# Performance work log

Measured on AMD Instinct MI355X. Metric: run time of the kernel, lower is better.

## Reference

```python
import jax, jax.numpy as jnp
import numpy as np

DIM = 512
N_HEADS = 8
HEAD_DIM = DIM // N_HEADS


def rope_pos(T, head_dim, dtype=jnp.float32):
    inv_freq = 1.0 / (10000.0 ** (jnp.arange(0, head_dim, 2, dtype=jnp.float32) / head_dim))
    t = jnp.arange(T, dtype=jnp.float32)
    freqs = jnp.einsum('i,j->ij', t, inv_freq)            # [T, head_dim/2]
    return jnp.concatenate([freqs, freqs], axis=-1).astype(dtype)  # [T, head_dim]


def rotate_half(x):
    x1, x2 = jnp.split(x, 2, axis=-1)
    return jnp.concatenate([-x2, x1], axis=-1)


def apply_rope(pos, t):
    # pos: [T, hd] -> broadcast to [1,1,T,hd]; t: [B,H,T,hd]
    pos = pos[None, None, :, :]
    return t * jnp.cos(pos) + rotate_half(t) * jnp.sin(pos)


def setup_inputs() -> dict:
    key = jax.random.key(0)
    ks = jax.random.split(key, 6)
    B, T = 4, 2048
    x = jax.random.normal(ks[0], (B, T, DIM), dtype=jnp.float32)
    mask = jnp.zeros((B, T), dtype=jnp.float32)  # additive mask
    s = 1.0 / np.sqrt(DIM)
    qkv_w = jax.random.normal(ks[1], (3 * DIM, DIM), dtype=jnp.float32) * s
    qkv_b = jnp.zeros((3 * DIM,), dtype=jnp.float32)
    proj_w = jax.random.normal(ks[2], (DIM, DIM), dtype=jnp.float32) * s
    proj_b = jnp.zeros((DIM,), dtype=jnp.float32)
    return {"x": x, "mask": mask, "qkv_w": qkv_w, "qkv_b": qkv_b,
            "proj_w": proj_w, "proj_b": proj_b}


def reference(x, mask, qkv_w, qkv_b, proj_w, proj_b):
    B, T, C = x.shape
    qkv = x @ qkv_w.T + qkv_b                       # [B,T,3C]
    qkv = qkv.reshape(B, T, 3, N_HEADS, HEAD_DIM)
    q, k, v = qkv[:, :, 0], qkv[:, :, 1], qkv[:, :, 2]  # [B,T,H,hd]
    q = q.transpose(0, 2, 1, 3)                     # [B,H,T,hd]
    k = k.transpose(0, 2, 1, 3)
    v = v.transpose(0, 2, 1, 3)
    pos = rope_pos(T, HEAD_DIM, x.dtype)
    q = apply_rope(pos, q)
    k = apply_rope(pos, k)
    scores = jnp.einsum('bhqd,bhkd->bhqk', q, k) * (1.0 / np.sqrt(HEAD_DIM))
    scores = scores + mask[:, None, None, :]        # 2D mask -> [B,1,1,T]
    probs = jax.nn.softmax(scores.astype(jnp.float32), axis=-1).astype(x.dtype)
    # dropout is identity in eval mode
    out = jnp.einsum('bhqk,bhkd->bhqd', probs, v)   # [B,H,T,hd]
    out = out.transpose(0, 2, 1, 3).reshape(B, T, C)
    return out @ proj_w.T + proj_b
```

## Files before the change

### kernel.cpp

```cpp
#include <hip/hip_runtime.h>
#include <math.h>


typedef __attribute__((ext_vector_type(8))) short bf16x8;
typedef __attribute__((ext_vector_type(4))) float floatx4;

#define LOG2E 1.44269504088896f
#define MAX3(a, b, c) fmaxf(fmaxf((a), (b)), (c))

__device__ __forceinline__ unsigned short f2bf(float f) {
  unsigned int u = __float_as_uint(f);
  u += 0x7fffu + ((u >> 16) & 1u);
  return (unsigned short)(u >> 16);
}

__device__ __forceinline__ unsigned int cvtpk_bf16(float a, float b) {
  unsigned int r;
  asm("v_cvt_pk_bf16_f32 %0, %1, %2" : "=v"(r) : "v"(a), "v"(b));
  return r;
}

__device__ __forceinline__ void gld_lds16(unsigned short* lds, const unsigned short* g) {
  __builtin_amdgcn_global_load_lds(
      (const __attribute__((address_space(1))) unsigned int*)g,
      (__attribute__((address_space(3))) unsigned int*)lds, 16, 0, 0);
}

__global__ __launch_bounds__(256) void prep_kernel(
    const float* __restrict__ x, const float* __restrict__ wq, const float* __restrict__ wp,
    const float* __restrict__ mask,
    unsigned short* __restrict__ xb, unsigned short* __restrict__ wqb,
    unsigned short* __restrict__ wpb, float* __restrict__ cosT, float* __restrict__ sinT,
    float* __restrict__ maskE) {
  int i = blockIdx.x * 256 + threadIdx.x;
  if (i < 655360) {
    int base = i * 8;
    const float* src;
    unsigned short* dst;
    int j;
    if (base < 4194304)      { src = x;  dst = xb;  j = base; }
    else if (base < 4980736) { src = wq; dst = wqb; j = base - 4194304; }
    else                     { src = wp; dst = wpb; j = base - 4980736; }
    float4 a = *(const float4*)(src + j);
    float4 b = *(const float4*)(src + j + 4);
    uint4 r;
    r.x = cvtpk_bf16(a.x, a.y);
    r.y = cvtpk_bf16(a.z, a.w);
    r.z = cvtpk_bf16(b.x, b.y);
    r.w = cvtpk_bf16(b.z, b.w);
    *(uint4*)(dst + j) = r;
  } else if (i < 720896) {
    int j = i - 655360;
    int t = j >> 5, f = j & 31;
    double fr = (double)t * pow(10000.0, -(double)f / 32.0);
    cosT[j] = (float)cos(fr);
    sinT[j] = (float)sin(fr);
  } else if (i < 721920) {
    int j = (i - 720896) * 8;
    float4 a = *(const float4*)(mask + j);
    float4 b = *(const float4*)(mask + j + 4);
    a.x *= LOG2E; a.y *= LOG2E; a.z *= LOG2E; a.w *= LOG2E;
    b.x *= LOG2E; b.y *= LOG2E; b.z *= LOG2E; b.w *= LOG2E;
    *(float4*)(maskE + j) = a;
    *(float4*)(maskE + j + 4) = b;
  }
}

__global__ __launch_bounds__(256) void qkv_kernel(
    const unsigned short* __restrict__ xb, const unsigned short* __restrict__ wqb,
    const float* __restrict__ qkv_b, const float* __restrict__ cosT,
    const float* __restrict__ sinT, unsigned short* __restrict__ Qb,
    unsigned short* __restrict__ Kb, unsigned short* __restrict__ Vtb) {
  __shared__ __align__(16) unsigned short SM[2][2][128 * 32];
  const int tid = threadIdx.x;
  const int wave = tid >> 6, lane = tid & 63, ln = lane & 15, quad = lane >> 4;
  const int m0 = blockIdx.x * 128, n0 = blockIdx.y * 128;
  const int wr = (wave >> 1) * 64, wc = (wave & 1) * 64;

  floatx4 acc[4][4];
#pragma unroll
  for (int i = 0; i < 4; ++i)
#pragma unroll
    for (int j = 0; j < 4; ++j) acc[i][j] = (floatx4){0.f, 0.f, 0.f, 0.f};

  const int c0 = tid, c1 = tid + 256;
  const int ar0 = c0 >> 2, ak0 = (c0 & 3) * 8;
  const int ar1 = c1 >> 2, ak1 = (c1 & 3) * 8;

  gld_lds16(SM[0][0] + c0 * 8, xb + (size_t)(m0 + ar0) * 512 + ak0);
  gld_lds16(SM[0][0] + c1 * 8, xb + (size_t)(m0 + ar1) * 512 + ak1);
  gld_lds16(SM[0][1] + c0 * 8, wqb + (size_t)(n0 + ar0) * 512 + ak0);
  gld_lds16(SM[0][1] + c1 * 8, wqb + (size_t)(n0 + ar1) * 512 + ak1);
  __syncthreads();

  for (int kt = 0; kt < 16; ++kt) {
    const int cur = kt & 1;
    if (kt < 15) {
      const int kn = (kt + 1) * 32;
      gld_lds16(SM[cur ^ 1][0] + c0 * 8, xb + (size_t)(m0 + ar0) * 512 + kn + ak0);
      gld_lds16(SM[cur ^ 1][0] + c1 * 8, xb + (size_t)(m0 + ar1) * 512 + kn + ak1);
      gld_lds16(SM[cur ^ 1][1] + c0 * 8, wqb + (size_t)(n0 + ar0) * 512 + kn + ak0);
      gld_lds16(SM[cur ^ 1][1] + c1 * 8, wqb + (size_t)(n0 + ar1) * 512 + kn + ak1);
    }
    bf16x8 af[4], bfb[4];
#pragma unroll
    for (int mi = 0; mi < 4; ++mi)
      af[mi] = *(const bf16x8*)(SM[cur][0] + (wr + mi * 16 + ln) * 32 + quad * 8);
#pragma unroll
    for (int ni = 0; ni < 4; ++ni)
      bfb[ni] = *(const bf16x8*)(SM[cur][1] + (wc + ni * 16 + ln) * 32 + quad * 8);
#pragma unroll
    for (int mi = 0; mi < 4; ++mi)
#pragma unroll
      for (int ni = 0; ni < 4; ++ni)
        acc[mi][ni] = __builtin_amdgcn_mfma_f32_16x16x32_bf16(af[mi], bfb[ni], acc[mi][ni], 0, 0, 0);
    __syncthreads();
  }

  const int colbase = n0 + wc;
  const int mat = colbase >> 9;
  float bias[4];
#pragma unroll
  for (int ni = 0; ni < 4; ++ni) bias[ni] = qkv_b[colbase + ni * 16 + ln];

  unsigned short* Ls = &SM[0][0][0];
  const int bidx = m0 >> 11, tl0 = m0 & 2047;
  const int h0 = (n0 & 511) >> 6;

  if (mat == 2) {
#pragma unroll
    for (int mi = 0; mi < 4; ++mi) {
      int r0 = wr + mi * 16 + quad * 4;
#pragma unroll
      for (int ni = 0; ni < 4; ++ni) {
        int c = wc + ni * 16 + ln;
        ushort4 pk;
        pk.x = f2bf(acc[mi][ni][0] + bias[ni]);
        pk.y = f2bf(acc[mi][ni][1] + bias[ni]);
        pk.z = f2bf(acc[mi][ni][2] + bias[ni]);
        pk.w = f2bf(acc[mi][ni][3] + bias[ni]);
        *(ushort4*)(Ls + c * 128 + (r0 ^ ((c & 7) << 3))) = pk;
      }
    }
    __syncthreads();
    const int j2 = tid & 15, rid = tid >> 4;
#pragma unroll
    for (int it = 0; it < 8; ++it) {
      int c = it * 16 + rid;
      int hh = c >> 6, dd = c & 63;
      uint4 v = *(const uint4*)(Ls + c * 128 + ((j2 * 8) ^ ((c & 7) << 3)));
      *(uint4*)(Vtb + ((size_t)(bidx * 8 + h0 + hh) * 64 + dd) * 2048 + tl0 + j2 * 8) = v;
    }
  } else {
    unsigned short* dst = (mat == 0) ? Qb : Kb;
    const float sc = (mat == 0) ? 0.125f * LOG2E : 1.0f;
#pragma unroll
    for (int mi = 0; mi < 4; ++mi) {
#pragma unroll
      for (int r = 0; r < 4; ++r) {
        int lr = wr + mi * 16 + quad * 4 + r;
        int t = tl0 + lr;
        const float* cr = cosT + t * 32;
        const float* sr = sinT + t * 32;
        int xr = (lr & 7) << 3;
#pragma unroll
        for (int ni = 0; ni < 2; ++ni) {
          int dlo = ni * 16 + ln;
          float cv = cr[dlo], sv = sr[dlo];
          float xlo = acc[mi][ni][r] + bias[ni];
          float xhi = acc[mi][ni + 2][r] + bias[ni + 2];
          Ls[lr * 128 + ((wc + dlo) ^ xr)]      = f2bf((xlo * cv - xhi * sv) * sc);
          Ls[lr * 128 + ((wc + dlo + 32) ^ xr)] = f2bf((xhi * cv + xlo * sv) * sc);
        }
      }
    }
    __syncthreads();
    const int jj = tid & 7, rowid = tid >> 3;
#pragma unroll
    for (int it = 0; it < 8; ++it) {
      int hr = it * 32 + rowid;
      int rr = hr & 127, hh = hr >> 7;
      int c = hh * 64 + jj * 8;
      uint4 v = *(const uint4*)(Ls + rr * 128 + (c ^ ((rr & 7) << 3)));
      *(uint4*)(dst + ((size_t)(bidx * 8 + h0 + hh) * 2048 + tl0 + rr) * 64 + jj * 8) = v;
    }
  }
}

__global__ __launch_bounds__(512) void attn_kernel(
    const unsigned short* __restrict__ Qb, const unsigned short* __restrict__ Kb,
    const unsigned short* __restrict__ Vtb, const float* __restrict__ maskE,
    unsigned short* __restrict__ attnb) {
  __shared__ __align__(16) unsigned short Ks[2][64 * 64];
  __shared__ __align__(16) unsigned short Vs[2][64 * 64];
  __shared__ __align__(16) unsigned short Ps[128 * 64];

  const int tid = threadIdx.x;
  const int wave = tid >> 6, lane = tid & 63, ln = lane & 15, quad = lane >> 4;
  const int swz = (ln & 7) << 3;
  const int bh = blockIdx.y;
  const int b = bh >> 3, h = bh & 7;
  const int q0 = blockIdx.x * 128;
  const int wq = wave * 16;

  const unsigned short* Qhead = Qb + (size_t)bh * 2048 * 64;
  const unsigned short* Khead = Kb + (size_t)bh * 2048 * 64;
  const unsigned short* Vhead = Vtb + (size_t)bh * 64 * 2048;

  bf16x8 qf[2];
#pragma unroll
  for (int ks = 0; ks < 2; ++ks)
    qf[ks] = *(const bf16x8*)(Qhead + (size_t)(q0 + wq + ln) * 64 + ks * 32 + quad * 8);

  floatx4 o[4];
#pragma unroll
  for (int mi2 = 0; mi2 < 4; ++mi2) o[mi2] = (floatx4){0.f, 0.f, 0.f, 0.f};
  float mrun = -INFINITY;
  float lrun = 0.f;

  const int srow = tid >> 3;
  const int gcol = (((tid & 7) ^ (srow & 7)) << 3);
  const unsigned short* ksrc = Khead + (size_t)srow * 64 + gcol;
  const unsigned short* vsrc = Vhead + (size_t)srow * 2048 + gcol;
  unsigned short* kdst0 = Ks[0] + tid * 8;
  unsigned short* vdst0 = Vs[0] + tid * 8;
  unsigned short* kdst1 = Ks[1] + tid * 8;
  unsigned short* vdst1 = Vs[1] + tid * 8;

  gld_lds16(kdst0, ksrc);
  gld_lds16(vdst0, vsrc);
  __syncthreads();

  for (int kt = 0; kt < 32; ++kt) {
    const int cur = kt & 1;
    const int k0 = kt * 64;
    if (kt < 31) {
      gld_lds16(cur ? kdst0 : kdst1, ksrc + (size_t)(k0 + 64) * 64);
      gld_lds16(cur ? vdst0 : vdst1, vsrc + k0 + 64);
    }

    floatx4 sm[4];
    __builtin_amdgcn_s_setprio(1);
#pragma unroll
    for (int mi = 0; mi < 4; ++mi) {
      bf16x8 kf0 = *(const bf16x8*)(Ks[cur] + (mi * 16 + ln) * 64 + ((quad * 8) ^ swz));
      bf16x8 kf1 = *(const bf16x8*)(Ks[cur] + (mi * 16 + ln) * 64 + ((32 + quad * 8) ^ swz));
      floatx4 a = (floatx4){0.f, 0.f, 0.f, 0.f};
      a = __builtin_amdgcn_mfma_f32_16x16x32_bf16(kf0, qf[0], a, 0, 0, 0);
      a = __builtin_amdgcn_mfma_f32_16x16x32_bf16(kf1, qf[1], a, 0, 0, 0);
      sm[mi] = a;
    }
    __builtin_amdgcn_s_setprio(0);
#pragma unroll
    for (int mi = 0; mi < 4; ++mi) {
      float4 mv = *(const float4*)(maskE + b * 2048 + k0 + mi * 16 + quad * 4);
      sm[mi][0] += mv.x; sm[mi][1] += mv.y;
      sm[mi][2] += mv.z; sm[mi][3] += mv.w;
    }
    float t0 = MAX3(sm[0][0], sm[0][1], sm[0][2]);
    float t1 = MAX3(sm[0][3], sm[1][0], sm[1][1]);
    float t2 = MAX3(sm[1][2], sm[1][3], sm[2][0]);
    float t3 = MAX3(sm[2][1], sm[2][2], sm[2][3]);
    float t4 = MAX3(sm[3][0], sm[3][1], sm[3][2]);
    float vmax = fmaxf(MAX3(t0, t1, t2), MAX3(t3, t4, sm[3][3]));
    vmax = fmaxf(vmax, __shfl_xor(vmax, 16));
    vmax = fmaxf(vmax, __shfl_xor(vmax, 32));
    if (__any(vmax > mrun)) {
      float nm = fmaxf(mrun, vmax);
      float alpha = exp2f(mrun - nm);
      mrun = nm;
      lrun *= alpha;
#pragma unroll
      for (int mi2 = 0; mi2 < 4; ++mi2) {
        o[mi2][0] *= alpha; o[mi2][1] *= alpha;
        o[mi2][2] *= alpha; o[mi2][3] *= alpha;
      }
    }
    float ps[4];
#pragma unroll
    for (int mi = 0; mi < 4; ++mi) {
      float p0 = exp2f(sm[mi][0] - mrun);
      float p1 = exp2f(sm[mi][1] - mrun);
      float p2 = exp2f(sm[mi][2] - mrun);
      float p3 = exp2f(sm[mi][3] - mrun);
      sm[mi][0] = p0; sm[mi][1] = p1; sm[mi][2] = p2; sm[mi][3] = p3;
      ps[mi] = (p0 + p1) + (p2 + p3);
    }
    float psum = (ps[0] + ps[1]) + (ps[2] + ps[3]);
    psum += __shfl_xor(psum, 16);
    psum += __shfl_xor(psum, 32);
    lrun += psum;

#pragma unroll
    for (int mi = 0; mi < 4; ++mi) {
      uint2 pk;
      pk.x = cvtpk_bf16(sm[mi][0], sm[mi][1]);
      pk.y = cvtpk_bf16(sm[mi][2], sm[mi][3]);
      *(uint2*)(Ps + (wq + ln) * 64 + ((mi * 16 + quad * 4) ^ swz)) = pk;
    }
    __builtin_amdgcn_s_setprio(1);
#pragma unroll
    for (int ks = 0; ks < 2; ++ks) {
      bf16x8 pb = *(const bf16x8*)(Ps + (wq + ln) * 64 + ((ks * 32 + quad * 8) ^ swz));
#pragma unroll
      for (int mi2 = 0; mi2 < 4; ++mi2) {
        bf16x8 vf = *(const bf16x8*)(Vs[cur] + (mi2 * 16 + ln) * 64 + ((ks * 32 + quad * 8) ^ swz));
        o[mi2] = __builtin_amdgcn_mfma_f32_16x16x32_bf16(vf, pb, o[mi2], 0, 0, 0);
      }
    }
    __builtin_amdgcn_s_setprio(0);

    __syncthreads();
  }

  {
    float inv = 1.f / lrun;
    int t = q0 + wq + ln;
    size_t base = ((size_t)b * 2048 + t) * 512 + h * 64;
#pragma unroll
    for (int mi2 = 0; mi2 < 4; ++mi2) {
      uint2 pk;
      pk.x = cvtpk_bf16(o[mi2][0] * inv, o[mi2][1] * inv);
      pk.y = cvtpk_bf16(o[mi2][2] * inv, o[mi2][3] * inv);
      *(uint2*)(attnb + base + mi2 * 16 + quad * 4) = pk;
    }
  }
}

__global__ __launch_bounds__(512) void proj_kernel(
    const unsigned short* __restrict__ ab, const unsigned short* __restrict__ wpb,
    const float* __restrict__ proj_b, float* __restrict__ out) {
  __shared__ __align__(16) unsigned short As[2][128 * 32];
  __shared__ __align__(16) unsigned short Bs[2][128 * 32];
  const int tid = threadIdx.x;
  const int wave = tid >> 6, lane = tid & 63, ln = lane & 15, quad = lane >> 4;
  const int m0 = blockIdx.x * 128, n0 = blockIdx.y * 128;
  const int wr = (wave >> 1) * 32, wc = (wave & 1) * 64;

  floatx4 acc[2][4];
#pragma unroll
  for (int i = 0; i < 2; ++i)
#pragma unroll
    for (int j = 0; j < 4; ++j) acc[i][j] = (floatx4){0.f, 0.f, 0.f, 0.f};

  const int ar = tid >> 2, ak = (tid & 3) * 8;

  gld_lds16(As[0] + tid * 8, ab + (size_t)(m0 + ar) * 512 + ak);
  gld_lds16(Bs[0] + tid * 8, wpb + (size_t)(n0 + ar) * 512 + ak);
  __syncthreads();

  for (int kt = 0; kt < 16; ++kt) {
    const int cur = kt & 1;
    if (kt < 15) {
      const int kn = (kt + 1) * 32;
      gld_lds16(As[cur ^ 1] + tid * 8, ab + (size_t)(m0 + ar) * 512 + kn + ak);
      gld_lds16(Bs[cur ^ 1] + tid * 8, wpb + (size_t)(n0 + ar) * 512 + kn + ak);
    }
    bf16x8 af[2], bfb[4];
#pragma unroll
    for (int mi = 0; mi < 2; ++mi)
      af[mi] = *(const bf16x8*)(As[cur] + (wr + mi * 16 + ln) * 32 + quad * 8);
#pragma unroll
    for (int ni = 0; ni < 4; ++ni)
      bfb[ni] = *(const bf16x8*)(Bs[cur] + (wc + ni * 16 + ln) * 32 + quad * 8);
#pragma unroll
    for (int mi = 0; mi < 2; ++mi)
#pragma unroll
      for (int ni = 0; ni < 4; ++ni)
        acc[mi][ni] = __builtin_amdgcn_mfma_f32_16x16x32_bf16(af[mi], bfb[ni], acc[mi][ni], 0, 0, 0);
    __syncthreads();
  }

#pragma unroll
  for (int mi = 0; mi < 2; ++mi)
#pragma unroll
    for (int ni = 0; ni < 4; ++ni) {
      int col = n0 + wc + ni * 16 + ln;
      float pb = proj_b[col];
#pragma unroll
      for (int r = 0; r < 4; ++r) {
        int row = m0 + wr + mi * 16 + quad * 4 + r;
        out[(size_t)row * 512 + col] = acc[mi][ni][r] + pb;
      }
    }
}

extern "C" void kernel_launch(void* const* d_in, const int* in_sizes, int n_in,
                              void* d_out, int out_size, void* d_ws, size_t ws_size,
                              hipStream_t stream) {
  const float* x      = (const float*)d_in[0];
  const float* mask   = (const float*)d_in[1];
  const float* qkv_w  = (const float*)d_in[2];
  const float* qkv_b  = (const float*)d_in[3];
  const float* proj_w = (const float*)d_in[4];
  const float* proj_b = (const float*)d_in[5];
  float* out = (float*)d_out;

  char* ws = (char*)d_ws;
  unsigned short* xb   = (unsigned short*)(ws);
  unsigned short* wqb  = (unsigned short*)(ws + 8388608);
  unsigned short* wpb  = (unsigned short*)(ws + 9961472);
  float* cosT          = (float*)(ws + 10485760);
  float* sinT          = (float*)(ws + 10747904);
  unsigned short* Qb   = (unsigned short*)(ws + 11010048);
  unsigned short* Kb   = (unsigned short*)(ws + 19398656);
  unsigned short* Vtb  = (unsigned short*)(ws + 27787264);
  unsigned short* attnb= (unsigned short*)(ws + 36175872);
  float* maskE         = (float*)(ws + 44564480);

  prep_kernel<<<2820, 256, 0, stream>>>(x, qkv_w, proj_w, mask, xb, wqb, wpb, cosT, sinT, maskE);
  dim3 g1(64, 12);
  qkv_kernel<<<g1, 256, 0, stream>>>(xb, wqb, qkv_b, cosT, sinT, Qb, Kb, Vtb);
  dim3 g2(16, 32);
  attn_kernel<<<g2, 512, 0, stream>>>(Qb, Kb, Vtb, maskE, attnb);
  dim3 g3(64, 4);
  proj_kernel<<<g3, 512, 0, stream>>>(attnb, wpb, proj_b, out);
}
```

Measured before the change: 187.1 us.

## Give each attention wave 32 query rows and register-staged K/V prefetch

```diff
diff --git a/kernel.cpp b/kernel.cpp
--- a/kernel.cpp
+++ b/kernel.cpp
@@ -187,7 +187,7 @@
   }
 }
 
-__global__ __launch_bounds__(512) void attn_kernel(
+__global__ __launch_bounds__(256) void attn_kernel(
     const unsigned short* __restrict__ Qb, const unsigned short* __restrict__ Kb,
     const unsigned short* __restrict__ Vtb, const float* __restrict__ maskE,
     unsigned short* __restrict__ attnb) {
@@ -201,127 +201,166 @@
   const int bh = blockIdx.y;
   const int b = bh >> 3, h = bh & 7;
   const int q0 = blockIdx.x * 128;
-  const int wq = wave * 16;
+  const int wq = wave * 32;
 
   const unsigned short* Qhead = Qb + (size_t)bh * 2048 * 64;
   const unsigned short* Khead = Kb + (size_t)bh * 2048 * 64;
   const unsigned short* Vhead = Vtb + (size_t)bh * 64 * 2048;
 
-  bf16x8 qf[2];
-#pragma unroll
-  for (int ks = 0; ks < 2; ++ks)
-    qf[ks] = *(const bf16x8*)(Qhead + (size_t)(q0 + wq + ln) * 64 + ks * 32 + quad * 8);
-
-  floatx4 o[4];
-#pragma unroll
-  for (int mi2 = 0; mi2 < 4; ++mi2) o[mi2] = (floatx4){0.f, 0.f, 0.f, 0.f};
-  float mrun = -INFINITY;
-  float lrun = 0.f;
+  bf16x8 qf[2][2];
+#pragma unroll
+  for (int ni2 = 0; ni2 < 2; ++ni2)
+#pragma unroll
+    for (int ks = 0; ks < 2; ++ks)
+      qf[ni2][ks] = *(const bf16x8*)(Qhead + (size_t)(q0 + wq + ni2 * 16 + ln) * 64 + ks * 32 + quad * 8);
+
+  floatx4 o[4][2];
+#pragma unroll
+  for (int mi2 = 0; mi2 < 4; ++mi2)
+#pragma unroll
+    for (int ni2 = 0; ni2 < 2; ++ni2) o[mi2][ni2] = (floatx4){0.f, 0.f, 0.f, 0.f};
+  float mrun[2] = {-INFINITY, -INFINITY};
+  float lrun[2] = {0.f, 0.f};
 
   const int srow = tid >> 3;
-  const int gcol = (((tid & 7) ^ (srow & 7)) << 3);
-  const unsigned short* ksrc = Khead + (size_t)srow * 64 + gcol;
-  const unsigned short* vsrc = Vhead + (size_t)srow * 2048 + gcol;
-  unsigned short* kdst0 = Ks[0] + tid * 8;
-  unsigned short* vdst0 = Vs[0] + tid * 8;
-  unsigned short* kdst1 = Ks[1] + tid * 8;
-  unsigned short* vdst1 = Vs[1] + tid * 8;
-
-  gld_lds16(kdst0, ksrc);
-  gld_lds16(vdst0, vsrc);
+  const int scol = (tid & 7) * 8;
+  const int sx = scol ^ ((srow & 7) << 3);
+  const int sd0 = srow * 64 + sx, sd1 = (srow + 32) * 64 + sx;
+
+  {
+    uint4 k0a = *(const uint4*)(Khead + (size_t)srow * 64 + scol);
+    uint4 k0b = *(const uint4*)(Khead + (size_t)(srow + 32) * 64 + scol);
+    uint4 v0a = *(const uint4*)(Vhead + (size_t)srow * 2048 + scol);
+    uint4 v0b = *(const uint4*)(Vhead + (size_t)(srow + 32) * 2048 + scol);
+    *(uint4*)(Ks[0] + sd0) = k0a;
+    *(uint4*)(Ks[0] + sd1) = k0b;
+    *(uint4*)(Vs[0] + sd0) = v0a;
+    *(uint4*)(Vs[0] + sd1) = v0b;
+  }
   __syncthreads();
 
   for (int kt = 0; kt < 32; ++kt) {
     const int cur = kt & 1;
     const int k0 = kt * 64;
+    uint4 kpa, kpb, vpa, vpb;
     if (kt < 31) {
-      gld_lds16(cur ? kdst0 : kdst1, ksrc + (size_t)(k0 + 64) * 64);
-      gld_lds16(cur ? vdst0 : vdst1, vsrc + k0 + 64);
-    }
-
-    floatx4 sm[4];
-    __builtin_amdgcn_s_setprio(1);
+      kpa = *(const uint4*)(Khead + (size_t)(k0 + 64 + srow) * 64 + scol);
+      kpb = *(const uint4*)(Khead + (size_t)(k0 + 64 + srow + 32) * 64 + scol);
+      vpa = *(const uint4*)(Vhead + (size_t)srow * 2048 + k0 + 64 + scol);
+      vpb = *(const uint4*)(Vhead + (size_t)(srow + 32) * 2048 + k0 + 64 + scol);
+    }
+
+    floatx4 sm[4][2];
 #pragma unroll
     for (int mi = 0; mi < 4; ++mi) {
       bf16x8 kf0 = *(const bf16x8*)(Ks[cur] + (mi * 16 + ln) * 64 + ((quad * 8) ^ swz));
       bf16x8 kf1 = *(const bf16x8*)(Ks[cur] + (mi * 16 + ln) * 64 + ((32 + quad * 8) ^ swz));
-      floatx4 a = (floatx4){0.f, 0.f, 0.f, 0.f};
-      a = __builtin_amdgcn_mfma_f32_16x16x32_bf16(kf0, qf[0], a, 0, 0, 0);
-      a = __builtin_amdgcn_mfma_f32_16x16x32_bf16(kf1, qf[1], a, 0, 0, 0);
-      sm[mi] = a;
-    }
-    __builtin_amdgcn_s_setprio(0);
+#pragma unroll
+      for (int ni2 = 0; ni2 < 2; ++ni2) {
+        floatx4 a = (floatx4){0.f, 0.f, 0.f, 0.f};
+        a = __builtin_amdgcn_mfma_f32_16x16x32_bf16(kf0, qf[ni2][0], a, 0, 0, 0);
+        a = __builtin_amdgcn_mfma_f32_16x16x32_bf16(kf1, qf[ni2][1], a, 0, 0, 0);
+        sm[mi][ni2] = a;
+      }
+    }
 #pragma unroll
     for (int mi = 0; mi < 4; ++mi) {
       float4 mv = *(const float4*)(maskE + b * 2048 + k0 + mi * 16 + quad * 4);
-      sm[mi][0] += mv.x; sm[mi][1] += mv.y;
-      sm[mi][2] += mv.z; sm[mi][3] += mv.w;
-    }
-    float t0 = MAX3(sm[0][0], sm[0][1], sm[0][2]);
-    float t1 = MAX3(sm[0][3], sm[1][0], sm[1][1]);
-    float t2 = MAX3(sm[1][2], sm[1][3], sm[2][0]);
-    float t3 = MAX3(sm[2][1], sm[2][2], sm[2][3]);
-    float t4 = MAX3(sm[3][0], sm[3][1], sm[3][2]);
-    float vmax = fmaxf(MAX3(t0, t1, t2), MAX3(t3, t4, sm[3][3]));
-    vmax = fmaxf(vmax, __shfl_xor(vmax, 16));
-    vmax = fmaxf(vmax, __shfl_xor(vmax, 32));
-    if (__any(vmax > mrun)) {
-      float nm = fmaxf(mrun, vmax);
-      float alpha = exp2f(mrun - nm);
-      mrun = nm;
-      lrun *= alpha;
-#pragma unroll
-      for (int mi2 = 0; mi2 < 4; ++mi2) {
-        o[mi2][0] *= alpha; o[mi2][1] *= alpha;
-        o[mi2][2] *= alpha; o[mi2][3] *= alpha;
-      }
-    }
-    float ps[4];
-#pragma unroll
-    for (int mi = 0; mi < 4; ++mi) {
-      float p0 = exp2f(sm[mi][0] - mrun);
-      float p1 = exp2f(sm[mi][1] - mrun);
-      float p2 = exp2f(sm[mi][2] - mrun);
-      float p3 = exp2f(sm[mi][3] - mrun);
-      sm[mi][0] = p0; sm[mi][1] = p1; sm[mi][2] = p2; sm[mi][3] = p3;
-      ps[mi] = (p0 + p1) + (p2 + p3);
-    }
-    float psum = (ps[0] + ps[1]) + (ps[2] + ps[3]);
-    psum += __shfl_xor(psum, 16);
-    psum += __shfl_xor(psum, 32);
-    lrun += psum;
-
-#pragma unroll
-    for (int mi = 0; mi < 4; ++mi) {
-      uint2 pk;
-      pk.x = cvtpk_bf16(sm[mi][0], sm[mi][1]);
-      pk.y = cvtpk_bf16(sm[mi][2], sm[mi][3]);
-      *(uint2*)(Ps + (wq + ln) * 64 + ((mi * 16 + quad * 4) ^ swz)) = pk;
-    }
-    __builtin_amdgcn_s_setprio(1);
+#pragma unroll
+      for (int ni2 = 0; ni2 < 2; ++ni2) {
+        sm[mi][ni2][0] += mv.x; sm[mi][ni2][1] += mv.y;
+        sm[mi][ni2][2] += mv.z; sm[mi][ni2][3] += mv.w;
+      }
+    }
+    float vmax[2];
+#pragma unroll
+    for (int ni2 = 0; ni2 < 2; ++ni2) {
+      float t0 = MAX3(sm[0][ni2][0], sm[0][ni2][1], sm[0][ni2][2]);
+      float t1 = MAX3(sm[0][ni2][3], sm[1][ni2][0], sm[1][ni2][1]);
+      float t2 = MAX3(sm[1][ni2][2], sm[1][ni2][3], sm[2][ni2][0]);
+      float t3 = MAX3(sm[2][ni2][1], sm[2][ni2][2], sm[2][ni2][3]);
+      float t4 = MAX3(sm[3][ni2][0], sm[3][ni2][1], sm[3][ni2][2]);
+      float vm = fmaxf(MAX3(t0, t1, t2), MAX3(t3, t4, sm[3][ni2][3]));
+      vm = fmaxf(vm, __shfl_xor(vm, 16));
+      vm = fmaxf(vm, __shfl_xor(vm, 32));
+      vmax[ni2] = vm;
+    }
+    if (__any((vmax[0] > mrun[0]) || (vmax[1] > mrun[1]))) {
+#pragma unroll
+      for (int ni2 = 0; ni2 < 2; ++ni2) {
+        float nm = fmaxf(mrun[ni2], vmax[ni2]);
+        float alpha = exp2f(mrun[ni2] - nm);
+        mrun[ni2] = nm;
+        lrun[ni2] *= alpha;
+#pragma unroll
+        for (int mi2 = 0; mi2 < 4; ++mi2) {
+          o[mi2][ni2][0] *= alpha; o[mi2][ni2][1] *= alpha;
+          o[mi2][ni2][2] *= alpha; o[mi2][ni2][3] *= alpha;
+        }
+      }
+    }
+#pragma unroll
+    for (int ni2 = 0; ni2 < 2; ++ni2) {
+      float ps[4];
+#pragma unroll
+      for (int mi = 0; mi < 4; ++mi) {
+        float p0 = exp2f(sm[mi][ni2][0] - mrun[ni2]);
+        float p1 = exp2f(sm[mi][ni2][1] - mrun[ni2]);
+        float p2 = exp2f(sm[mi][ni2][2] - mrun[ni2]);
+        float p3 = exp2f(sm[mi][ni2][3] - mrun[ni2]);
+        sm[mi][ni2][0] = p0; sm[mi][ni2][1] = p1;
+        sm[mi][ni2][2] = p2; sm[mi][ni2][3] = p3;
+        ps[mi] = (p0 + p1) + (p2 + p3);
+      }
+      float psum = (ps[0] + ps[1]) + (ps[2] + ps[3]);
+      psum += __shfl_xor(psum, 16);
+      psum += __shfl_xor(psum, 32);
+      lrun[ni2] += psum;
+    }
+
+#pragma unroll
+    for (int mi = 0; mi < 4; ++mi)
+#pragma unroll
+      for (int ni2 = 0; ni2 < 2; ++ni2) {
+        uint2 pk;
+        pk.x = cvtpk_bf16(sm[mi][ni2][0], sm[mi][ni2][1]);
+        pk.y = cvtpk_bf16(sm[mi][ni2][2], sm[mi][ni2][3]);
+        *(uint2*)(Ps + (wq + ni2 * 16 + ln) * 64 + ((mi * 16 + quad * 4) ^ swz)) = pk;
+      }
 #pragma unroll
     for (int ks = 0; ks < 2; ++ks) {
-      bf16x8 pb = *(const bf16x8*)(Ps + (wq + ln) * 64 + ((ks * 32 + quad * 8) ^ swz));
+      bf16x8 pb[2];
+#pragma unroll
+      for (int ni2 = 0; ni2 < 2; ++ni2)
+        pb[ni2] = *(const bf16x8*)(Ps + (wq + ni2 * 16 + ln) * 64 + ((ks * 32 + quad * 8) ^ swz));
 #pragma unroll
       for (int mi2 = 0; mi2 < 4; ++mi2) {
         bf16x8 vf = *(const bf16x8*)(Vs[cur] + (mi2 * 16 + ln) * 64 + ((ks * 32 + quad * 8) ^ swz));
-        o[mi2] = __builtin_amdgcn_mfma_f32_16x16x32_bf16(vf, pb, o[mi2], 0, 0, 0);
-      }
-    }
-    __builtin_amdgcn_s_setprio(0);
-
-    __syncthreads();
-  }
-
-  {
-    float inv = 1.f / lrun;
-    int t = q0 + wq + ln;
+#pragma unroll
+        for (int ni2 = 0; ni2 < 2; ++ni2)
+          o[mi2][ni2] = __builtin_amdgcn_mfma_f32_16x16x32_bf16(vf, pb[ni2], o[mi2][ni2], 0, 0, 0);
+      }
+    }
+
+    if (kt < 31) {
+      *(uint4*)(Ks[cur ^ 1] + sd0) = kpa;
+      *(uint4*)(Ks[cur ^ 1] + sd1) = kpb;
+      *(uint4*)(Vs[cur ^ 1] + sd0) = vpa;
+      *(uint4*)(Vs[cur ^ 1] + sd1) = vpb;
+      __syncthreads();
+    }
+  }
+
+#pragma unroll
+  for (int ni2 = 0; ni2 < 2; ++ni2) {
+    float inv = 1.f / lrun[ni2];
+    int t = q0 + wq + ni2 * 16 + ln;
     size_t base = ((size_t)b * 2048 + t) * 512 + h * 64;
 #pragma unroll
     for (int mi2 = 0; mi2 < 4; ++mi2) {
       uint2 pk;
-      pk.x = cvtpk_bf16(o[mi2][0] * inv, o[mi2][1] * inv);
-      pk.y = cvtpk_bf16(o[mi2][2] * inv, o[mi2][3] * inv);
+      pk.x = cvtpk_bf16(o[mi2][ni2][0] * inv, o[mi2][ni2][1] * inv);
+      pk.y = cvtpk_bf16(o[mi2][ni2][2] * inv, o[mi2][ni2][3] * inv);
       *(uint2*)(attnb + base + mi2 * 16 + quad * 4) = pk;
     }
   }
@@ -412,7 +451,7 @@
   dim3 g1(64, 12);
   qkv_kernel<<<g1, 256, 0, stream>>>(xb, wqb, qkv_b, cosT, sinT, Qb, Kb, Vtb);
   dim3 g2(16, 32);
-  attn_kernel<<<g2, 512, 0, stream>>>(Qb, Kb, Vtb, maskE, attnb);
+  attn_kernel<<<g2, 256, 0, stream>>>(Qb, Kb, Vtb, maskE, attnb);
   dim3 g3(64, 4);
   proj_kernel<<<g3, 512, 0, stream>>>(attnb, wpb, proj_b, out);
 }
```

After: 199.9 us. +6.8%, slower.

## Register-staged K/V prefetch in attention, drop setprio, smaller proj tiles

Applied to the files above, without the earlier changes.

```diff
diff --git a/kernel.cpp b/kernel.cpp
--- a/kernel.cpp
+++ b/kernel.cpp
@@ -219,28 +219,27 @@
   float lrun = 0.f;
 
   const int srow = tid >> 3;
-  const int gcol = (((tid & 7) ^ (srow & 7)) << 3);
-  const unsigned short* ksrc = Khead + (size_t)srow * 64 + gcol;
-  const unsigned short* vsrc = Vhead + (size_t)srow * 2048 + gcol;
-  unsigned short* kdst0 = Ks[0] + tid * 8;
-  unsigned short* vdst0 = Vs[0] + tid * 8;
-  unsigned short* kdst1 = Ks[1] + tid * 8;
-  unsigned short* vdst1 = Vs[1] + tid * 8;
-
-  gld_lds16(kdst0, ksrc);
-  gld_lds16(vdst0, vsrc);
+  const int scol = (tid & 7) * 8;
+  const int sdst = srow * 64 + (scol ^ ((srow & 7) << 3));
+
+  {
+    uint4 k0v = *(const uint4*)(Khead + (size_t)srow * 64 + scol);
+    uint4 v0v = *(const uint4*)(Vhead + (size_t)srow * 2048 + scol);
+    *(uint4*)(Ks[0] + sdst) = k0v;
+    *(uint4*)(Vs[0] + sdst) = v0v;
+  }
   __syncthreads();
 
   for (int kt = 0; kt < 32; ++kt) {
     const int cur = kt & 1;
     const int k0 = kt * 64;
+    uint4 kpre, vpre;
     if (kt < 31) {
-      gld_lds16(cur ? kdst0 : kdst1, ksrc + (size_t)(k0 + 64) * 64);
-      gld_lds16(cur ? vdst0 : vdst1, vsrc + k0 + 64);
+      kpre = *(const uint4*)(Khead + (size_t)(k0 + 64 + srow) * 64 + scol);
+      vpre = *(const uint4*)(Vhead + (size_t)srow * 2048 + k0 + 64 + scol);
     }
 
     floatx4 sm[4];
-    __builtin_amdgcn_s_setprio(1);
 #pragma unroll
     for (int mi = 0; mi < 4; ++mi) {
       bf16x8 kf0 = *(const bf16x8*)(Ks[cur] + (mi * 16 + ln) * 64 + ((quad * 8) ^ swz));
@@ -250,7 +249,6 @@
       a = __builtin_amdgcn_mfma_f32_16x16x32_bf16(kf1, qf[1], a, 0, 0, 0);
       sm[mi] = a;
     }
-    __builtin_amdgcn_s_setprio(0);
 #pragma unroll
     for (int mi = 0; mi < 4; ++mi) {
       float4 mv = *(const float4*)(maskE + b * 2048 + k0 + mi * 16 + quad * 4);
@@ -298,7 +296,6 @@
       pk.y = cvtpk_bf16(sm[mi][2], sm[mi][3]);
       *(uint2*)(Ps + (wq + ln) * 64 + ((mi * 16 + quad * 4) ^ swz)) = pk;
     }
-    __builtin_amdgcn_s_setprio(1);
 #pragma unroll
     for (int ks = 0; ks < 2; ++ks) {
       bf16x8 pb = *(const bf16x8*)(Ps + (wq + ln) * 64 + ((ks * 32 + quad * 8) ^ swz));
@@ -308,9 +305,12 @@
         o[mi2] = __builtin_amdgcn_mfma_f32_16x16x32_bf16(vf, pb, o[mi2], 0, 0, 0);
       }
     }
-    __builtin_amdgcn_s_setprio(0);
-
-    __syncthreads();
+
+    if (kt < 31) {
+      *(uint4*)(Ks[cur ^ 1] + sdst) = kpre;
+      *(uint4*)(Vs[cur ^ 1] + sdst) = vpre;
+      __syncthreads();
+    }
   }
 
   {
@@ -327,21 +327,21 @@
   }
 }
 
-__global__ __launch_bounds__(512) void proj_kernel(
+__global__ __launch_bounds__(256) void proj_kernel(
     const unsigned short* __restrict__ ab, const unsigned short* __restrict__ wpb,
     const float* __restrict__ proj_b, float* __restrict__ out) {
-  __shared__ __align__(16) unsigned short As[2][128 * 32];
-  __shared__ __align__(16) unsigned short Bs[2][128 * 32];
+  __shared__ __align__(16) unsigned short As[2][64 * 32];
+  __shared__ __align__(16) unsigned short Bs[2][64 * 32];
   const int tid = threadIdx.x;
   const int wave = tid >> 6, lane = tid & 63, ln = lane & 15, quad = lane >> 4;
-  const int m0 = blockIdx.x * 128, n0 = blockIdx.y * 128;
-  const int wr = (wave >> 1) * 32, wc = (wave & 1) * 64;
-
-  floatx4 acc[2][4];
+  const int m0 = blockIdx.x * 64, n0 = blockIdx.y * 64;
+  const int wr = (wave >> 1) * 32, wc = (wave & 1) * 32;
+
+  floatx4 acc[2][2];
 #pragma unroll
   for (int i = 0; i < 2; ++i)
 #pragma unroll
-    for (int j = 0; j < 4; ++j) acc[i][j] = (floatx4){0.f, 0.f, 0.f, 0.f};
+    for (int j = 0; j < 2; ++j) acc[i][j] = (floatx4){0.f, 0.f, 0.f, 0.f};
 
   const int ar = tid >> 2, ak = (tid & 3) * 8;
 
@@ -356,17 +356,17 @@
       gld_lds16(As[cur ^ 1] + tid * 8, ab + (size_t)(m0 + ar) * 512 + kn + ak);
       gld_lds16(Bs[cur ^ 1] + tid * 8, wpb + (size_t)(n0 + ar) * 512 + kn + ak);
     }
-    bf16x8 af[2], bfb[4];
+    bf16x8 af[2], bfb[2];
 #pragma unroll
     for (int mi = 0; mi < 2; ++mi)
       af[mi] = *(const bf16x8*)(As[cur] + (wr + mi * 16 + ln) * 32 + quad * 8);
 #pragma unroll
-    for (int ni = 0; ni < 4; ++ni)
+    for (int ni = 0; ni < 2; ++ni)
       bfb[ni] = *(const bf16x8*)(Bs[cur] + (wc + ni * 16 + ln) * 32 + quad * 8);
 #pragma unroll
     for (int mi = 0; mi < 2; ++mi)
 #pragma unroll
-      for (int ni = 0; ni < 4; ++ni)
+      for (int ni = 0; ni < 2; ++ni)
         acc[mi][ni] = __builtin_amdgcn_mfma_f32_16x16x32_bf16(af[mi], bfb[ni], acc[mi][ni], 0, 0, 0);
     __syncthreads();
   }
@@ -374,7 +374,7 @@
 #pragma unroll
   for (int mi = 0; mi < 2; ++mi)
 #pragma unroll
-    for (int ni = 0; ni < 4; ++ni) {
+    for (int ni = 0; ni < 2; ++ni) {
       int col = n0 + wc + ni * 16 + ln;
       float pb = proj_b[col];
 #pragma unroll
@@ -413,6 +413,6 @@
   qkv_kernel<<<g1, 256, 0, stream>>>(xb, wqb, qkv_b, cosT, sinT, Qb, Kb, Vtb);
   dim3 g2(16, 32);
   attn_kernel<<<g2, 512, 0, stream>>>(Qb, Kb, Vtb, maskE, attnb);
-  dim3 g3(64, 4);
-  proj_kernel<<<g3, 512, 0, stream>>>(attnb, wpb, proj_b, out);
-}
+  dim3 g3(128, 8);
+  proj_kernel<<<g3, 256, 0, stream>>>(attnb, wpb, proj_b, out);
+}
```

Result: no change. 184.2 us (-1.5%).
